# Performance work log

Hardware: AMD Instinct MI355X
Metric: run time of the kernel (lower is better)

Reference implementation:

```python
import jax, jax.numpy as jnp
import numpy as np

N_NODES = 20000
N_EDGES = 320000
IN_FEATS = 64
HIDDENS = [128, 128, 128]
K = 4        # n_kernels
DIM = 2      # pseudo_coord


def setup_inputs() -> dict:
    key = jax.random.key(0)
    ks = jax.random.split(key, 32)
    inp = {
        "features": jax.random.normal(ks[0], (N_NODES, IN_FEATS), dtype=jnp.float32),
        "pseudo": jax.random.uniform(ks[1], (N_EDGES, DIM), dtype=jnp.float32),
        "src": jax.random.randint(ks[2], (N_EDGES,), 0, N_NODES, dtype=jnp.int32),
        "dst": jax.random.randint(ks[3], (N_EDGES,), 0, N_NODES, dtype=jnp.int32),
    }
    dims_in = [IN_FEATS] + HIDDENS[:-1]
    ki = 4
    for i, (din, dout) in enumerate(zip(dims_in, HIDDENS)):
        inp[f"fc_w{i}"] = jax.random.normal(ks[ki], (din, K * dout), dtype=jnp.float32) * (1.0 / np.sqrt(din)); ki += 1
        inp[f"mu{i}"] = jax.random.normal(ks[ki], (K, DIM), dtype=jnp.float32) * 0.1; ki += 1
        inp[f"inv_sigma{i}"] = jnp.ones((K, DIM), dtype=jnp.float32)
        inp[f"bias{i}"] = jnp.zeros((dout,), dtype=jnp.float32)
        inp[f"pw{i}"] = jax.random.normal(ks[ki], (DIM, DIM), dtype=jnp.float32) * 0.5; ki += 1
        inp[f"pb{i}"] = jnp.zeros((DIM,), dtype=jnp.float32)
    return inp


def _gmm_layer(h, pseudo, src, dst, fc_w, mu, inv_sigma, bias, pw, pb):
    k, dim = mu.shape
    dout = fc_w.shape[1] // k
    hp = (h @ fc_w).reshape(-1, k, dout)              # [N, K, out]
    u = jnp.tanh(pseudo @ pw + pb)                    # [E, dim] per-layer pseudo projection
    diff = (u[:, None, :] - mu[None, :, :]) * inv_sigma[None, :, :]
    w = jnp.exp(-0.5 * jnp.sum(diff * diff, axis=-1))  # [E, K] Gaussian mixture weights
    msg = jnp.einsum('ek,eko->eo', w, hp[src])         # gather + weighted mix -> [E, out]
    agg = jax.ops.segment_sum(msg, dst, num_segments=h.shape[0])  # scatter-sum
    return agg + bias


def reference(features, pseudo, src, dst,
              fc_w0, mu0, inv_sigma0, bias0, pw0, pb0,
              fc_w1, mu1, inv_sigma1, bias1, pw1, pb1,
              fc_w2, mu2, inv_sigma2, bias2, pw2, pb2):
    h = features
    h = _gmm_layer(h, pseudo, src, dst, fc_w0, mu0, inv_sigma0, bias0, pw0, pb0)
    h = _gmm_layer(h, pseudo, src, dst, fc_w1, mu1, inv_sigma1, bias1, pw1, pb1)
    h = _gmm_layer(h, pseudo, src, dst, fc_w2, mu2, inv_sigma2, bias2, pw2, pb2)
    return h
```

## Files before the change

### kernel.cpp

```cpp
#include <hip/hip_runtime.h>
#include <hip/hip_bf16.h>
#include <hip/hip_fp16.h>
#include <math.h>

#define NN 20000
#define NE 320000
#define SLOT 64

typedef __attribute__((ext_vector_type(8))) _Float16 f16x8;
typedef __attribute__((ext_vector_type(2))) _Float16 h16x2;
typedef __attribute__((ext_vector_type(4))) float f32x4;

__device__ inline ushort f2h(float f) {
    __half h = __float2half_rn(f);
    return *reinterpret_cast<ushort*>(&h);
}
__device__ inline uint pack2h(float a, float b) {
    return (uint)f2h(a) | ((uint)f2h(b) << 16);
}
__device__ inline h16x2 u2h2(uint x) {
    union { uint u; h16x2 h; } c; c.u = x; return c.h;
}
__device__ inline uint pack_lo(uint x, uint y) {
    return __builtin_amdgcn_perm(x, y, 0x01000504u);
}
__device__ inline uint pack_hi(uint x, uint y) {
    return __builtin_amdgcn_perm(x, y, 0x03020706u);
}

__device__ inline float fast_tanh(float x) {
    x = fminf(fmaxf(x, -9.f), 9.f);
    float e = __expf(2.f * x);
    return 1.f - 2.f / (e + 1.f);
}

struct EdgeParams {
    const float *pw0, *pb0, *mu0, *is0;
    const float *pw1, *pb1, *mu1, *is1;
    const float *pw2, *pb2, *mu2, *is2;
};

__device__ inline void layer_w(float p0, float p1, const float* pw, const float* pb,
                               const float* mu, const float* is, float* out4) {
    float u0 = fast_tanh(p0 * pw[0] + p1 * pw[2] + pb[0]);
    float u1 = fast_tanh(p0 * pw[1] + p1 * pw[3] + pb[1]);
#pragma unroll
    for (int k = 0; k < 4; ++k) {
        float d0 = (u0 - mu[k * 2 + 0]) * is[k * 2 + 0];
        float d1 = (u1 - mu[k * 2 + 1]) * is[k * 2 + 1];
        out4[k] = __expf(-0.5f * (d0 * d0 + d1 * d1));
    }
}

__global__ void fill_prep(const int* __restrict__ dst, const int* __restrict__ src,
                          const float* __restrict__ pseudo, EdgeParams P,
                          int* __restrict__ cursor, uint* __restrict__ recs,
                          const float* __restrict__ features, ushort* __restrict__ fbf,
                          const float* __restrict__ f0, const float* __restrict__ f1,
                          const float* __restrict__ f2, ushort* __restrict__ w0,
                          ushort* __restrict__ w1, ushort* __restrict__ w2) {
    __shared__ float tile[64][65];
    int bid = blockIdx.x;
    if (bid < 1250) {
        int e = bid * 256 + threadIdx.x;
        int n = dst[e];
        int pos = atomicAdd(&cursor[n], 1);
        if (pos < SLOT) {
            size_t slot = (size_t)n * SLOT + pos;
            float2 p = *(const float2*)(pseudo + (size_t)e * 2);
            float w[4];
            uint pk0x, pk0y, pk1x, pk1y, pk2x, pk2y;
            layer_w(p.x, p.y, P.pw0, P.pb0, P.mu0, P.is0, w);
            pk0x = pack2h(w[0], w[1]);
            pk0y = pack2h(w[2], w[3]);
            layer_w(p.x, p.y, P.pw1, P.pb1, P.mu1, P.is1, w);
            pk1x = pack2h(w[0], w[1]);
            pk1y = pack2h(w[2], w[3]);
            layer_w(p.x, p.y, P.pw2, P.pb2, P.mu2, P.is2, w);
            pk2x = pack2h(w[0], w[1]);
            pk2y = pack2h(w[2], w[3]);
            uint* r = recs + slot * 8;
            *(uint4*)(r + 0) = make_uint4((uint)src[e], 0u, pk0x, pk0y);
            *(uint4*)(r + 4) = make_uint4(pk1x, pk1y, pk2x, pk2y);
        }
    } else if (bid < 1290) {
        int b = bid - 1250;
        const float* srcp;
        ushort* dstp;
        int din, KD, k, nt, dt;
        if (b < 8)       { srcp = f0; dstp = w0; din = 64;  KD = 256; k = b >> 1; nt = b & 1; dt = 0; }
        else if (b < 24) { int t = b - 8;  srcp = f1; dstp = w1; din = 128; KD = 512; k = t >> 2; nt = (t >> 1) & 1; dt = t & 1; }
        else             { int t = b - 24; srcp = f2; dstp = w2; din = 128; KD = 512; k = t >> 2; nt = (t >> 1) & 1; dt = t & 1; }
        int n0 = nt * 64, d0 = dt * 64;
        int tx = threadIdx.x & 63, ty = threadIdx.x >> 6;
#pragma unroll
        for (int ii = 0; ii < 16; ++ii) {
            int dr = ty * 16 + ii;
            tile[dr][tx] = srcp[(size_t)(d0 + dr) * 512 + k * 128 + n0 + tx];
        }
        __syncthreads();
#pragma unroll
        for (int ii = 0; ii < 16; ++ii) {
            int nr = ty * 16 + ii;
            dstp[(size_t)(n0 + nr) * KD + k * din + d0 + tx] = f2h(tile[tx][nr]);
        }
    } else {
        int idx = (bid - 1290) * 256 + threadIdx.x;
        size_t b8 = (size_t)idx * 8;
        float4 a = *(const float4*)(features + b8);
        float4 b = *(const float4*)(features + b8 + 4);
        uint4 o;
        o.x = pack2h(a.x, a.y);
        o.y = pack2h(a.z, a.w);
        o.z = pack2h(b.x, b.y);
        o.w = pack2h(b.z, b.w);
        *(uint4*)(fbf + b8) = o;
    }
}

template <int DIN, bool OUTF16>
__global__ __launch_bounds__(1024, 8) void layer_fused(
    const ushort* __restrict__ hbf, const int* __restrict__ cursor,
    const uint* __restrict__ recs, int woff,
    const ushort* __restrict__ Bt, const float* __restrict__ bias,
    void* __restrict__ hout) {
    constexpr int KD = 4 * DIN;
    constexpr int PITCH = KD + 8;
    constexpr int B = 8;
    constexpr int FPL = DIN / 32;
    __shared__ __align__(16) ushort Ts[16 * PITCH];
    __shared__ __align__(16) f32x4 red[8][64];
    int wv = threadIdx.x >> 6, lane = threadIdx.x & 63;
    int l16 = lane & 15, quad = lane >> 4;
    int half = lane >> 5, l32 = lane & 31;
    int nb = blockIdx.x * 16;
    int n = nb + wv;

    {
        int deg = __builtin_amdgcn_readfirstlane(cursor[n]);
        deg = deg < SLOT ? deg : SLOT;
        size_t base = (size_t)n * SLOT;

        float acc[4 * FPL];
#pragma unroll
        for (int j = 0; j < 4 * FPL; ++j) acc[j] = 0.f;

        {
            int s[B];
            uint wlo[B], whi[B];
            uint2 hv[B];
#pragma unroll
            for (int u = 0; u < B; ++u) {
                size_t idx = base + 2 * u + half;
                const uint* r = recs + idx * 8;
                int sv = (int)r[0];
                uint2 wp = *(const uint2*)(r + woff);
                bool ok = (2 * u + half) < deg;
                s[u] = ok ? sv : 0;
                wlo[u] = ok ? wp.x : 0u;
                whi[u] = ok ? wp.y : 0u;
            }
#pragma unroll
            for (int u = 0; u < B; ++u) {
                const ushort* rowp = hbf + (size_t)s[u] * DIN + l32 * FPL;
                if (DIN == 64)
                    hv[u].x = *(const uint*)rowp;
                else
                    hv[u] = *(const uint2*)rowp;
            }
#pragma unroll
            for (int u = 0; u < B; u += 2) {
                uint wp0 = pack_lo(wlo[u], wlo[u + 1]);
                uint wp1 = pack_hi(wlo[u], wlo[u + 1]);
                uint wp2 = pack_lo(whi[u], whi[u + 1]);
                uint wp3 = pack_hi(whi[u], whi[u + 1]);
                h16x2 w2[4] = {u2h2(wp0), u2h2(wp1), u2h2(wp2), u2h2(wp3)};
                h16x2 f2[FPL];
                f2[0] = u2h2(pack_lo(hv[u].x, hv[u + 1].x));
                f2[1] = u2h2(pack_hi(hv[u].x, hv[u + 1].x));
                if (DIN == 128) {
                    f2[2] = u2h2(pack_lo(hv[u].y, hv[u + 1].y));
                    f2[3] = u2h2(pack_hi(hv[u].y, hv[u + 1].y));
                }
#pragma unroll
                for (int k = 0; k < 4; ++k)
#pragma unroll
                    for (int j = 0; j < FPL; ++j)
                        acc[k * FPL + j] = __builtin_amdgcn_fdot2(
                            w2[k], f2[j], acc[k * FPL + j], false);
            }
        }
        for (int i = 16; i < deg; i += 2 * B) {
            int s[B];
            uint wlo[B], whi[B];
            uint2 hv[B];
#pragma unroll
            for (int u = 0; u < B; ++u) {
                int ii = i + 2 * u + half;
                bool ok = ii < deg;
                size_t idx = base + (ok ? ii : 0);
                const uint* r = recs + idx * 8;
                s[u] = (int)r[0];
                uint2 wp = *(const uint2*)(r + woff);
                wlo[u] = ok ? wp.x : 0u;
                whi[u] = ok ? wp.y : 0u;
            }
#pragma unroll
            for (int u = 0; u < B; ++u) {
                const ushort* rowp = hbf + (size_t)s[u] * DIN + l32 * FPL;
                if (DIN == 64)
                    hv[u].x = *(const uint*)rowp;
                else
                    hv[u] = *(const uint2*)rowp;
            }
#pragma unroll
            for (int u = 0; u < B; u += 2) {
                uint wp0 = pack_lo(wlo[u], wlo[u + 1]);
                uint wp1 = pack_hi(wlo[u], wlo[u + 1]);
                uint wp2 = pack_lo(whi[u], whi[u + 1]);
                uint wp3 = pack_hi(whi[u], whi[u + 1]);
                h16x2 w2[4] = {u2h2(wp0), u2h2(wp1), u2h2(wp2), u2h2(wp3)};
                h16x2 f2[FPL];
                f2[0] = u2h2(pack_lo(hv[u].x, hv[u + 1].x));
                f2[1] = u2h2(pack_hi(hv[u].x, hv[u + 1].x));
                if (DIN == 128) {
                    f2[2] = u2h2(pack_lo(hv[u].y, hv[u + 1].y));
                    f2[3] = u2h2(pack_hi(hv[u].y, hv[u + 1].y));
                }
#pragma unroll
                for (int k = 0; k < 4; ++k)
#pragma unroll
                    for (int j = 0; j < FPL; ++j)
                        acc[k * FPL + j] = __builtin_amdgcn_fdot2(
                            w2[k], f2[j], acc[k * FPL + j], false);
            }
        }
#pragma unroll
        for (int j = 0; j < 4 * FPL; ++j) acc[j] += __shfl_xor(acc[j], 32);

        if (half == 0) {
#pragma unroll
            for (int k = 0; k < 4; ++k) {
                if (DIN == 64) {
                    ushort2 p;
                    p.x = f2h(acc[k * 2 + 0]);
                    p.y = f2h(acc[k * 2 + 1]);
                    *(ushort2*)(Ts + wv * PITCH + k * DIN + l32 * 2) = p;
                } else {
                    ushort4 p;
                    p.x = f2h(acc[k * 4 + 0]);
                    p.y = f2h(acc[k * 4 + 1]);
                    p.z = f2h(acc[k * 4 + 2]);
                    p.w = f2h(acc[k * 4 + 3]);
                    *(ushort4*)(Ts + wv * PITCH + k * DIN + l32 * 4) = p;
                }
            }
        }
    }
    __syncthreads();

    {
        constexpr int KH = KD / 2;
        int kh = wv >> 3;
        int ct = wv & 7;
        int c0 = ct * 16;
        f32x4 accg = (f32x4){0.f, 0.f, 0.f, 0.f};
        int kbeg = kh * KH;
#pragma unroll 4
        for (int k0 = kbeg; k0 < kbeg + KH; k0 += 32) {
            f16x8 af = *(const f16x8*)(Ts + l16 * PITCH + k0 + quad * 8);
            f16x8 bfr = *(const f16x8*)(Bt + (size_t)(c0 + l16) * KD + k0 + quad * 8);
            accg = __builtin_amdgcn_mfma_f32_16x16x32_f16(af, bfr, accg, 0, 0, 0);
        }
        if (kh == 1) red[ct][lane] = accg;
        __syncthreads();
        if (kh == 0) {
            f32x4 other = red[ct][lane];
            int gn = c0 + l16;
            float bv = bias[gn];
#pragma unroll
            for (int i = 0; i < 4; ++i) {
                int gm = nb + quad * 4 + i;
                float val = accg[i] + other[i] + bv;
                if (OUTF16)
                    ((ushort*)hout)[(size_t)gm * 128 + gn] = f2h(val);
                else
                    ((float*)hout)[(size_t)gm * 128 + gn] = val;
            }
        }
    }
}

extern "C" void kernel_launch(void* const* d_in, const int* in_sizes, int n_in,
                              void* d_out, int out_size, void* d_ws, size_t ws_size,
                              hipStream_t stream) {
    const float* features = (const float*)d_in[0];
    const float* pseudo = (const float*)d_in[1];
    const int* src = (const int*)d_in[2];
    const int* dst = (const int*)d_in[3];
    const float* fc_w[3] = {(const float*)d_in[4], (const float*)d_in[10], (const float*)d_in[16]};
    const float* mu[3] = {(const float*)d_in[5], (const float*)d_in[11], (const float*)d_in[17]};
    const float* isg[3] = {(const float*)d_in[6], (const float*)d_in[12], (const float*)d_in[18]};
    const float* bias[3] = {(const float*)d_in[7], (const float*)d_in[13], (const float*)d_in[19]};
    const float* pw[3] = {(const float*)d_in[8], (const float*)d_in[14], (const float*)d_in[20]};
    const float* pb[3] = {(const float*)d_in[9], (const float*)d_in[15], (const float*)d_in[21]};

    char* ws = (char*)d_ws;
    auto alloc = [&](size_t bytes) -> void* {
        void* p = (void*)ws;
        ws += (bytes + 255) & ~(size_t)255;
        return p;
    };
    int* cursor = (int*)alloc((size_t)NN * 4);
    uint* recs = (uint*)alloc((size_t)NN * SLOT * 32);
    ushort* fbf = (ushort*)alloc((size_t)NN * 64 * 2);
    ushort* w2t_0 = (ushort*)alloc((size_t)128 * 256 * 2);
    ushort* w2t_1 = (ushort*)alloc((size_t)128 * 512 * 2);
    ushort* w2t_2 = (ushort*)alloc((size_t)128 * 512 * 2);
    ushort* h1 = (ushort*)alloc((size_t)NN * 128 * 2);
    ushort* h2 = (ushort*)alloc((size_t)NN * 128 * 2);

    hipMemsetAsync(cursor, 0, (size_t)NN * 4, stream);
    EdgeParams P;
    P.pw0 = pw[0]; P.pb0 = pb[0]; P.mu0 = mu[0]; P.is0 = isg[0];
    P.pw1 = pw[1]; P.pb1 = pb[1]; P.mu1 = mu[1]; P.is1 = isg[1];
    P.pw2 = pw[2]; P.pb2 = pb[2]; P.mu2 = mu[2]; P.is2 = isg[2];
    fill_prep<<<1915, 256, 0, stream>>>(dst, src, pseudo, P, cursor, recs, features, fbf,
                                        fc_w[0], fc_w[1], fc_w[2], w2t_0, w2t_1, w2t_2);

    const int GB = NN / 16;

    layer_fused<64, true><<<GB, 1024, 0, stream>>>(
        fbf, cursor, recs, 2, w2t_0, bias[0], h1);
    layer_fused<128, true><<<GB, 1024, 0, stream>>>(
        h1, cursor, recs, 4, w2t_1, bias[1], h2);
    layer_fused<128, false><<<GB, 1024, 0, stream>>>(
        h2, cursor, recs, 6, w2t_2, bias[2], (float*)d_out);
}
```

Before: 223.4 us.

## Sort nodes by in-degree so each block processes similar-degree nodes

Adds a single-block counting sort that buckets nodes by clamped in-degree into a permutation array. The three fused layer kernels then map each wave to a permuted node and write outputs through that permutation. The goal is to balance work among the 16 waves in a block so no block waits on one high-degree node. In exchange it adds an extra serial single-block kernel launch and scattered output writes with poorer locality for the gathered rows.

```diff
diff --git a/kernel.cpp b/kernel.cpp
--- a/kernel.cpp
+++ b/kernel.cpp
@@ -118,10 +118,37 @@
     }
 }
 
+__global__ __launch_bounds__(1024) void k_sort(const int* __restrict__ cursor,
+                                               int* __restrict__ perm) {
+    __shared__ int hist[65];
+    __shared__ int off[65];
+    int t = threadIdx.x;
+    if (t < 65) hist[t] = 0;
+    __syncthreads();
+    for (int n = t; n < NN; n += 1024) {
+        int d = cursor[n];
+        d = d < 64 ? d : 64;
+        atomicAdd(&hist[d < 64 ? d : 64], 1);
+    }
+    __syncthreads();
+    if (t == 0) {
+        int run = 0;
+#pragma unroll
+        for (int i = 0; i < 65; ++i) { off[i] = run; run += hist[i]; }
+    }
+    __syncthreads();
+    for (int n = t; n < NN; n += 1024) {
+        int d = cursor[n];
+        d = d < 64 ? d : 64;
+        int pos = atomicAdd(&off[d], 1);
+        perm[pos] = n;
+    }
+}
+
 template <int DIN, bool OUTF16>
 __global__ __launch_bounds__(1024, 8) void layer_fused(
     const ushort* __restrict__ hbf, const int* __restrict__ cursor,
-    const uint* __restrict__ recs, int woff,
+    const int* __restrict__ perm, const uint* __restrict__ recs, int woff,
     const ushort* __restrict__ Bt, const float* __restrict__ bias,
     void* __restrict__ hout) {
     constexpr int KD = 4 * DIN;
@@ -130,11 +157,13 @@
     constexpr int FPL = DIN / 32;
     __shared__ __align__(16) ushort Ts[16 * PITCH];
     __shared__ __align__(16) f32x4 red[8][64];
+    __shared__ int prow[16];
     int wv = threadIdx.x >> 6, lane = threadIdx.x & 63;
     int l16 = lane & 15, quad = lane >> 4;
     int half = lane >> 5, l32 = lane & 31;
     int nb = blockIdx.x * 16;
-    int n = nb + wv;
+    int n = __builtin_amdgcn_readfirstlane(perm[nb + wv]);
+    if (lane == 0) prow[wv] = n;
 
     {
         int deg = __builtin_amdgcn_readfirstlane(cursor[n]);
@@ -280,7 +309,7 @@
             float bv = bias[gn];
 #pragma unroll
             for (int i = 0; i < 4; ++i) {
-                int gm = nb + quad * 4 + i;
+                int gm = prow[quad * 4 + i];
                 float val = accg[i] + other[i] + bv;
                 if (OUTF16)
                     ((ushort*)hout)[(size_t)gm * 128 + gn] = f2h(val);
@@ -312,6 +341,7 @@
         return p;
     };
     int* cursor = (int*)alloc((size_t)NN * 4);
+    int* perm = (int*)alloc((size_t)NN * 4);
     uint* recs = (uint*)alloc((size_t)NN * SLOT * 32);
     ushort* fbf = (ushort*)alloc((size_t)NN * 64 * 2);
     ushort* w2t_0 = (ushort*)alloc((size_t)128 * 256 * 2);
@@ -327,13 +357,14 @@
     P.pw2 = pw[2]; P.pb2 = pb[2]; P.mu2 = mu[2]; P.is2 = isg[2];
     fill_prep<<<1915, 256, 0, stream>>>(dst, src, pseudo, P, cursor, recs, features, fbf,
                                         fc_w[0], fc_w[1], fc_w[2], w2t_0, w2t_1, w2t_2);
+    k_sort<<<1, 1024, 0, stream>>>(cursor, perm);
 
     const int GB = NN / 16;
 
     layer_fused<64, true><<<GB, 1024, 0, stream>>>(
-        fbf, cursor, recs, 2, w2t_0, bias[0], h1);
+        fbf, cursor, perm, recs, 2, w2t_0, bias[0], h1);
     layer_fused<128, true><<<GB, 1024, 0, stream>>>(
-        h1, cursor, recs, 4, w2t_1, bias[1], h2);
+        h1, cursor, perm, recs, 4, w2t_1, bias[1], h2);
     layer_fused<128, false><<<GB, 1024, 0, stream>>>(
-        h2, cursor, recs, 6, w2t_2, bias[2], (float*)d_out);
-}
+        h2, cursor, perm, recs, 6, w2t_2, bias[2], (float*)d_out);
+}
```

After: 236.5 us. 5.9% more time.
